# Performance work log

Measured on AMD Instinct MI355X. Metric: run time of the kernel, lower is better.

Reference implementation:

```python
import jax, jax.numpy as jnp
import numpy as np

T, B, D, H = 2048, 4, 1024, 16
DK = D // H
SCALE = 1.0 / np.sqrt(DK)


def setup_inputs() -> dict:
    key = jax.random.key(0)
    k1, k2, k3 = jax.random.split(key, 3)
    x = jax.random.normal(k1, (T, B, D), dtype=jnp.float32)
    # xavier_uniform-ish scaling
    W_qkv = jax.random.normal(k2, (3 * D, D), dtype=jnp.float32) * np.sqrt(2.0 / (D + 3 * D))
    W_out = jax.random.normal(k3, (D, D), dtype=jnp.float32) * np.sqrt(1.0 / D)
    b_out = jnp.zeros((D,), dtype=jnp.float32)
    return {"x": x, "W_qkv": W_qkv, "W_out": W_out, "b_out": b_out}


def reference(x, W_qkv, W_out, b_out):
    Tn, Bn, Dn = x.shape
    # QKV projection (Linear with weight [3D, D], no bias)
    qkv = x @ W_qkv.T                                  # (T, B, 3D)
    qkv = qkv.reshape(Tn, Bn, 3, H, DK)
    q, k, v = qkv[:, :, 0], qkv[:, :, 1], qkv[:, :, 2]  # each (T, B, H, dk)
    scores = jnp.einsum('tbhd,sbhd->bhts', q, k) * SCALE  # (B, H, T, T)
    causal = jnp.triu(jnp.ones((Tn, Tn), dtype=bool), k=1)
    scores = jnp.where(causal, -jnp.inf, scores)
    attn = jax.nn.softmax(scores, axis=-1)
    out = jnp.einsum('bhts,sbhd->tbhd', attn, v)        # (T, B, H, dk)
    out = out.reshape(Tn, Bn, Dn)
    return out @ W_out.T + b_out
```

## Files before the change

### kernel.cpp

```cpp
#include <hip/hip_runtime.h>
#include <stdint.h>

#define T_DIM 2048
#define B_DIM 4
#define D_DIM 1024
#define H_NUM 16
#define HD 64
#define MROWS (T_DIM * B_DIM)
#define QKV_N (3 * D_DIM)
#define ATT_C 0.18033688011112042f

typedef unsigned short u16;
typedef __bf16 bf16x8 __attribute__((ext_vector_type(8)));
typedef float f32x4 __attribute__((ext_vector_type(4)));
typedef float f32x16 __attribute__((ext_vector_type(16)));
typedef u16 u16x4 __attribute__((ext_vector_type(4)));
typedef u16 u16x8 __attribute__((ext_vector_type(8)));

__device__ __forceinline__ u16 f2bf(float f) {
  union { float f; unsigned u; } v; v.f = f;
  unsigned r = v.u + 0x7fffu + ((v.u >> 16) & 1u);
  return (u16)(r >> 16);
}

__device__ __forceinline__ void async_copy16(void* lds, const void* g) {
  __builtin_amdgcn_global_load_lds((__attribute__((address_space(1))) void*)(g),
                                   (__attribute__((address_space(3))) void*)(lds),
                                   16, 0, 0);
}

__global__ __launch_bounds__(256) void cast3_f32_bf16(
    const float* __restrict__ s0, const float* __restrict__ s1,
    const float* __restrict__ s2, u16* __restrict__ dst,
    int n0, int n01, int ntot4) {
  int i = blockIdx.x * 256 + threadIdx.x;
  if (i >= ntot4) return;
  int e = i * 4;
  const float* s; int off;
  if (e < n0) { s = s0; off = 0; }
  else if (e < n01) { s = s1; off = n0; }
  else { s = s2; off = n01; }
  float4 v = *reinterpret_cast<const float4*>(s + (e - off));
  u16x4 o = {f2bf(v.x), f2bf(v.y), f2bf(v.z), f2bf(v.w)};
  *reinterpret_cast<u16x4*>(dst + e) = o;
}

template <int OUT_F32_BIAS>
__global__ __launch_bounds__(256) void gemm_bt(
    const u16* __restrict__ A, const u16* __restrict__ Bm,
    u16* __restrict__ Cb, float* __restrict__ Cf, const float* __restrict__ bias,
    int M, int N, int K) {
  __shared__ __attribute__((aligned(16))) u16 As[128 * 64];
  __shared__ __attribute__((aligned(16))) u16 Bs[128 * 64];

  const int tid = threadIdx.x;
  const int lane = tid & 63, wid = tid >> 6;
  const int l15 = lane & 15, lg = lane >> 4;
  const int wr = wid >> 1, wc = wid & 1;
  const int m0 = blockIdx.y * 128, n0 = blockIdx.x * 128;

  f32x4 acc[4][4];
#pragma unroll
  for (int i = 0; i < 4; i++)
#pragma unroll
    for (int j = 0; j < 4; j++) acc[i][j] = (f32x4){0.f, 0.f, 0.f, 0.f};

  const int srow = tid >> 3;
  const int scol = (tid & 7) * 8;
  const u16* gA = A + (size_t)(m0 + srow) * K + scol;
  const u16* gB = Bm + (size_t)(n0 + srow) * K + scol;
  u16* lA = As + tid * 8;
  u16* lB = Bs + tid * 8;

  const int KT = K >> 6;
  for (int kt = 0; kt < KT; ++kt) {
    const int kofs = kt * 64;
#pragma unroll
    for (int p = 0; p < 4; ++p) {
      async_copy16(lA + p * 256 * 8, gA + (size_t)(p * 32) * K + kofs);
      async_copy16(lB + p * 256 * 8, gB + (size_t)(p * 32) * K + kofs);
    }
    __syncthreads();
#pragma unroll
    for (int kk = 0; kk < 2; ++kk) {
      bf16x8 af[4], bfr[4];
#pragma unroll
      for (int mt = 0; mt < 4; ++mt)
        af[mt] = *reinterpret_cast<const bf16x8*>(
            &As[(wr * 64 + mt * 16 + l15) * 64 + kk * 32 + lg * 8]);
#pragma unroll
      for (int nt = 0; nt < 4; ++nt)
        bfr[nt] = *reinterpret_cast<const bf16x8*>(
            &Bs[(wc * 64 + nt * 16 + l15) * 64 + kk * 32 + lg * 8]);
#pragma unroll
      for (int mt = 0; mt < 4; ++mt)
#pragma unroll
        for (int nt = 0; nt < 4; ++nt)
          acc[mt][nt] = __builtin_amdgcn_mfma_f32_16x16x32_bf16(
              af[mt], bfr[nt], acc[mt][nt], 0, 0, 0);
    }
    __syncthreads();
  }

#pragma unroll
  for (int mt = 0; mt < 4; ++mt) {
#pragma unroll
    for (int r = 0; r < 4; ++r) {
      const int row = m0 + wr * 64 + mt * 16 + lg * 4 + r;
#pragma unroll
      for (int nt = 0; nt < 4; ++nt) {
        const int col = n0 + wc * 64 + nt * 16 + l15;
        float v = acc[mt][nt][r];
        if (OUT_F32_BIAS) {
          Cf[(size_t)row * N + col] = v + bias[col];
        } else {
          Cb[(size_t)row * N + col] = f2bf(v);
        }
      }
    }
  }
}

__global__ __launch_bounds__(512, 1) void gemm_bt8_qkv(
    const u16* __restrict__ A, const u16* __restrict__ Bm,
    u16* __restrict__ Cb, int M, int N, int K) {
  extern __shared__ u16 sm[];

  const int tid = threadIdx.x;
  const int lane = tid & 63, wid = tid >> 6;
  const int wr = wid >> 2, wc = wid & 3;
  const int l15 = lane & 15, lg = lane >> 4;
  const int xr = ((l15 >> 2) & 1) << 4;

  const int nwg = gridDim.x * gridDim.y;
  const int lin = blockIdx.y * gridDim.x + blockIdx.x;
  const int swz = (lin & 7) * (nwg >> 3) + (lin >> 3);
  const int bx = swz % gridDim.x, by = swz / gridDim.x;
  const int m0 = by * 256, n0 = bx * 256;

  const int srow = tid >> 3;
  const int kxs = ((tid & 7) * 8) ^ (((tid >> 5) & 1) << 4);
  const u16* gA = A + (size_t)(m0 + srow) * K + kxs;
  const u16* gB = Bm + (size_t)(n0 + srow) * K + kxs;

#define STG(op_, h_, tk_, c_)                                                   \
  {                                                                             \
    const u16* g_ = ((op_) ? gB : gA) + (size_t)((h_) * 128) * K + (size_t)(tk_) * 64; \
    u16* d_ = sm + (c_) * 32768 + (op_) * 16384 + (h_) * 8192 + tid * 8;        \
    async_copy16(d_, g_);                                                       \
    async_copy16(d_ + 4096, g_ + (size_t)64 * K);                               \
  }

#define LDA_(mt_, kk_, c_)                                                      \
  (*reinterpret_cast<const bf16x8*>(sm + (c_) * 32768 + wr * 8192 +             \
      ((mt_) * 16 + l15) * 64 + (((kk_) * 32 + lg * 8) ^ xr)))
#define LDB_(nt_, kk_, c_)                                                      \
  (*reinterpret_cast<const bf16x8*>(sm + (c_) * 32768 + 16384 + (wc >> 1) * 8192 + \
      ((wc & 1) * 64 + (nt_) * 16 + l15) * 64 + (((kk_) * 32 + lg * 8) ^ xr)))

  f32x4 acc[8][4];
#pragma unroll
  for (int i = 0; i < 8; i++)
#pragma unroll
    for (int j = 0; j < 4; j++) acc[i][j] = (f32x4){0.f, 0.f, 0.f, 0.f};

  const int NT = K >> 6;

  STG(0, 0, 0, 0) STG(0, 1, 0, 0) STG(1, 0, 0, 0) STG(1, 1, 0, 0)
  STG(0, 0, 1, 1) STG(0, 1, 1, 1)
  asm volatile("s_waitcnt vmcnt(4)" ::: "memory");
  __builtin_amdgcn_sched_barrier(0);
  __builtin_amdgcn_s_barrier();

  for (int t = 0; t < NT; ++t) {
    const int c = t & 1;
    bf16x8 a03[4][2], a47[4][2], b01[2][2], b23[2][2];
#pragma unroll
    for (int mt = 0; mt < 4; ++mt) {
      a03[mt][0] = LDA_(mt, 0, c);
      a03[mt][1] = LDA_(mt, 1, c);
    }
#pragma unroll
    for (int nt = 0; nt < 2; ++nt) {
      b01[nt][0] = LDB_(nt, 0, c);
      b01[nt][1] = LDB_(nt, 1, c);
    }
    if (t + 1 < NT) STG(1, 0, t + 1, c ^ 1)
    __builtin_amdgcn_s_barrier();
    asm volatile("s_waitcnt lgkmcnt(0)" ::: "memory");
    __builtin_amdgcn_sched_barrier(0);
    __builtin_amdgcn_s_setprio(1);
#pragma unroll
    for (int mt = 0; mt < 4; ++mt)
#pragma unroll
      for (int nt = 0; nt < 2; ++nt)
#pragma unroll
        for (int kk = 0; kk < 2; ++kk)
          acc[mt][nt] = __builtin_amdgcn_mfma_f32_16x16x32_bf16(
              a03[mt][kk], b01[nt][kk], acc[mt][nt], 0, 0, 0);
    __builtin_amdgcn_s_setprio(0);
    __builtin_amdgcn_s_barrier();
#pragma unroll
    for (int mt = 0; mt < 4; ++mt) {
      a47[mt][0] = LDA_(mt + 4, 0, c);
      a47[mt][1] = LDA_(mt + 4, 1, c);
    }
    if (t + 1 < NT) STG(1, 1, t + 1, c ^ 1)
    __builtin_amdgcn_s_barrier();
    asm volatile("s_waitcnt lgkmcnt(0)" ::: "memory");
    __builtin_amdgcn_sched_barrier(0);
    __builtin_amdgcn_s_setprio(1);
#pragma unroll
    for (int mt = 0; mt < 4; ++mt)
#pragma unroll
      for (int nt = 0; nt < 2; ++nt)
#pragma unroll
        for (int kk = 0; kk < 2; ++kk)
          acc[mt + 4][nt] = __builtin_amdgcn_mfma_f32_16x16x32_bf16(
              a47[mt][kk], b01[nt][kk], acc[mt + 4][nt], 0, 0, 0);
    __builtin_amdgcn_s_setprio(0);
    __builtin_amdgcn_s_barrier();
#pragma unroll
    for (int nt = 0; nt < 2; ++nt) {
      b23[nt][0] = LDB_(nt + 2, 0, c);
      b23[nt][1] = LDB_(nt + 2, 1, c);
    }
    if (t + 2 < NT) STG(0, 0, t + 2, c)
    __builtin_amdgcn_s_barrier();
    asm volatile("s_waitcnt lgkmcnt(0)" ::: "memory");
    __builtin_amdgcn_sched_barrier(0);
    __builtin_amdgcn_s_setprio(1);
#pragma unroll
    for (int mt = 0; mt < 4; ++mt)
#pragma unroll
      for (int nt = 0; nt < 2; ++nt)
#pragma unroll
        for (int kk = 0; kk < 2; ++kk)
          acc[mt][nt + 2] = __builtin_amdgcn_mfma_f32_16x16x32_bf16(
              a03[mt][kk], b23[nt][kk], acc[mt][nt + 2], 0, 0, 0);
    __builtin_amdgcn_s_setprio(0);
    __builtin_amdgcn_s_barrier();
    if (t + 2 < NT) STG(0, 1, t + 2, c)
    __builtin_amdgcn_s_barrier();
    __builtin_amdgcn_s_setprio(1);
#pragma unroll
    for (int mt = 0; mt < 4; ++mt)
#pragma unroll
      for (int nt = 0; nt < 2; ++nt)
#pragma unroll
        for (int kk = 0; kk < 2; ++kk)
          acc[mt + 4][nt + 2] = __builtin_amdgcn_mfma_f32_16x16x32_bf16(
              a47[mt][kk], b23[nt][kk], acc[mt + 4][nt + 2], 0, 0, 0);
    __builtin_amdgcn_s_setprio(0);
    if (t + 1 < NT) {
      if (t + 2 < NT) {
        asm volatile("s_waitcnt vmcnt(4)" ::: "memory");
      } else {
        asm volatile("s_waitcnt vmcnt(0)" ::: "memory");
      }
      __builtin_amdgcn_sched_barrier(0);
    }
    __builtin_amdgcn_s_barrier();
  }

  const float qsc = (n0 < D_DIM) ? ATT_C : 1.0f;
#pragma unroll
  for (int mt = 0; mt < 8; ++mt) {
#pragma unroll
    for (int r = 0; r < 4; ++r) {
      const int row = m0 + wr * 128 + mt * 16 + lg * 4 + r;
#pragma unroll
      for (int nt = 0; nt < 4; ++nt) {
        const int col = n0 + wc * 64 + nt * 16 + l15;
        Cb[(size_t)row * N + col] = f2bf(acc[mt][nt][r] * qsc);
      }
    }
  }
#undef STG
#undef LDA_
#undef LDB_
}

#define VF_STRIDE 24
#define VF_FRAG (32 * VF_STRIDE)

__device__ __forceinline__ void process32(
    const bf16x8 (&qf)[4], f32x16 (&o)[2], f32x16& lacc,
    int q0w, int kv0, int l31, int hi, bool needMask, const bf16x8 onesf,
    const u16* __restrict__ Ks, const u16* __restrict__ Vf) {
  f32x16 s[2];
#pragma unroll
  for (int kb = 0; kb < 2; ++kb)
#pragma unroll
    for (int r = 0; r < 16; ++r) s[kb][r] = 0.f;

  __builtin_amdgcn_s_setprio(1);
#pragma unroll
  for (int kb = 0; kb < 2; ++kb) {
#pragma unroll
    for (int ks = 0; ks < 4; ++ks) {
      const int row = kb * 32 + l31;
      bf16x8 kf = *reinterpret_cast<const bf16x8*>(
          &Ks[row * 64 + ((((ks << 1) | hi)) ^ (l31 & 7)) * 8]);
      s[kb] = __builtin_amdgcn_mfma_f32_32x32x16_bf16(kf, qf[ks], s[kb], 0, 0, 0);
    }
  }
  __builtin_amdgcn_s_setprio(0);

  if (needMask) {
    const int q = q0w + l31;
#pragma unroll
    for (int kb = 0; kb < 2; ++kb)
#pragma unroll
      for (int r = 0; r < 16; ++r) {
        const int kv = kv0 + kb * 32 + (r & 3) + ((r >> 2) << 3) + (hi << 2);
        if (kv > q) s[kb][r] = -1e30f;
      }
  }
#pragma unroll
  for (int kb = 0; kb < 2; ++kb)
#pragma unroll
    for (int r = 0; r < 16; ++r)
      s[kb][r] = __builtin_amdgcn_exp2f(s[kb][r]);

  union Frag { unsigned u[4]; bf16x8 v; };
  Frag pf[4];
#pragma unroll
  for (int kb = 0; kb < 2; ++kb)
#pragma unroll
    for (int g = 0; g < 2; ++g) {
#pragma unroll
      for (int t2 = 0; t2 < 2; ++t2) {
        unsigned x, y;
        asm("v_cvt_pk_bf16_f32 %0, %1, %2"
            : "=v"(x) : "v"(s[kb][g * 8 + t2 * 2]), "v"(s[kb][g * 8 + t2 * 2 + 1]));
        asm("v_cvt_pk_bf16_f32 %0, %1, %2"
            : "=v"(y) : "v"(s[kb][g * 8 + t2 * 2 + 4]), "v"(s[kb][g * 8 + t2 * 2 + 5]));
        asm("v_permlane32_swap_b32 %0, %1" : "+v"(x), "+v"(y));
        pf[kb * 2 + g].u[t2] = x;
        pf[kb * 2 + g].u[t2 + 2] = y;
      }
    }

  __builtin_amdgcn_s_setprio(1);
#pragma unroll
  for (int ks = 0; ks < 4; ++ks) {
    lacc = __builtin_amdgcn_mfma_f32_32x32x16_bf16(onesf, pf[ks].v, lacc, 0, 0, 0);
#pragma unroll
    for (int db = 0; db < 2; ++db) {
      bf16x8 vf = *reinterpret_cast<const bf16x8*>(
          &Vf[(ks * 2 + db) * VF_FRAG + l31 * VF_STRIDE + hi * 8]);
      o[db] = __builtin_amdgcn_mfma_f32_32x32x16_bf16(vf, pf[ks].v, o[db], 0, 0, 0);
    }
  }
  __builtin_amdgcn_s_setprio(0);
}

__global__ __launch_bounds__(256, 2) void attn_kernel(
    const u16* __restrict__ qkv, u16* __restrict__ aout) {
  __shared__ __attribute__((aligned(16))) u16 Ks[128 * 64];
  __shared__ __attribute__((aligned(16))) u16 Vf[16 * VF_FRAG];

  const int tid = threadIdx.x;
  const int lane = tid & 63, w = tid >> 6;
  const int l31 = lane & 31, hi = lane >> 5;

  const int nwg = gridDim.x * gridDim.y;
  const int lin = blockIdx.y * gridDim.x + blockIdx.x;
  const int swz = (lin & 7) * (nwg >> 3) + (lin >> 3);
  const int px = swz % gridDim.x;
  const int bh = swz / gridDim.x;
  const int b = bh >> 4, h = bh & 15;
  const int qtA = px, qtB = 15 - px;
  const int q0A = qtA * 128 + w * 32, q0B = qtB * 128 + w * 32;

  bf16x8 qfA[4], qfB[4];
  {
    const u16* pA = qkv + ((size_t)(q0A + l31) * B_DIM + b) * QKV_N + h * HD + hi * 8;
    const u16* pB = qkv + ((size_t)(q0B + l31) * B_DIM + b) * QKV_N + h * HD + hi * 8;
#pragma unroll
    for (int ks = 0; ks < 4; ++ks) {
      qfA[ks] = *reinterpret_cast<const bf16x8*>(pA + ks * 16);
      qfB[ks] = *reinterpret_cast<const bf16x8*>(pB + ks * 16);
    }
  }

  bf16x8 onesf;
  {
    union { u16 u[8]; bf16x8 v; } ou;
#pragma unroll
    for (int i = 0; i < 8; ++i) ou.u[i] = 0x3F80;
    onesf = ou.v;
  }

  f32x16 oA[2], oB[2], laccA, laccB;
#pragma unroll
  for (int r = 0; r < 16; ++r) { laccA[r] = 0.f; laccB[r] = 0.f; }
#pragma unroll
  for (int db = 0; db < 2; ++db)
#pragma unroll
    for (int r = 0; r < 16; ++r) { oA[db][r] = 0.f; oB[db][r] = 0.f; }

  const int srow = tid >> 3;
  const int scol = (tid & 7) * 8;
  const int csw = (tid & 7) ^ (srow & 7);

  for (int kt2 = 0; kt2 <= qtB; ++kt2) {
    const int base = kt2 * 128;
#pragma unroll
    for (int p = 0; p < 4; ++p) {
      const u16* gK = qkv + ((size_t)(base + p * 32 + srow) * B_DIM + b) * QKV_N +
                      D_DIM + h * HD + csw * 8;
      async_copy16(Ks + tid * 8 + p * 2048, gK);
    }
    u16x8 vv[4];
#pragma unroll
    for (int p = 0; p < 4; ++p) {
      const u16* gV = qkv + ((size_t)(base + p * 32 + srow) * B_DIM + b) * QKV_N +
                      2 * D_DIM + h * HD + scol;
      vv[p] = *reinterpret_cast<const u16x8*>(gV);
    }
#pragma unroll
    for (int p = 0; p < 4; ++p) {
      const int kvl = p * 32 + srow;
      const int fb = (kvl >> 4) * 2;
      const int e16 = kvl & 15;
#pragma unroll
      for (int jj = 0; jj < 8; ++jj) {
        const int j = (jj + srow) & 7;
        const int d = scol + j;
        Vf[(fb + (d >> 5)) * VF_FRAG + (d & 31) * VF_STRIDE + e16] = vv[p][j];
      }
    }
    __syncthreads();

#pragma unroll
    for (int half = 0; half < 2; ++half) {
      const int kv0 = base + half * 64;
      const u16* Kh = Ks + half * (64 * 64);
      const u16* Vh = Vf + half * 8 * VF_FRAG;
      if (kv0 <= q0A + 31)
        process32(qfA, oA, laccA, q0A, kv0, l31, hi, kv0 + 63 > q0A, onesf, Kh, Vh);
      if (kv0 <= q0B + 31)
        process32(qfB, oB, laccB, q0B, kv0, l31, hi, kv0 + 63 > q0B, onesf, Kh, Vh);
    }
    __syncthreads();
  }

#pragma unroll
  for (int t = 0; t < 2; ++t) {
    const float inv = 1.0f / (t == 0 ? laccA[0] : laccB[0]);
    const int q0w = t == 0 ? q0A : q0B;
    f32x16* o = t == 0 ? oA : oB;
    u16* orow = aout + ((size_t)(q0w + l31) * B_DIM + b) * D_DIM + h * HD;
#pragma unroll
    for (int db = 0; db < 2; ++db)
#pragma unroll
      for (int rq = 0; rq < 4; ++rq) {
        u16x4 o4;
#pragma unroll
        for (int e = 0; e < 4; ++e) o4[e] = f2bf(o[db][rq * 4 + e] * inv);
        *reinterpret_cast<u16x4*>(orow + db * 32 + rq * 8 + hi * 4) = o4;
      }
  }
}

extern "C" void kernel_launch(void* const* d_in, const int* in_sizes, int n_in,
                              void* d_out, int out_size, void* d_ws, size_t ws_size,
                              hipStream_t stream) {
  (void)in_sizes; (void)n_in; (void)out_size; (void)ws_size;
  const float* x = (const float*)d_in[0];
  const float* Wqkv = (const float*)d_in[1];
  const float* Wout = (const float*)d_in[2];
  const float* bout = (const float*)d_in[3];
  float* out = (float*)d_out;

  u16* xb = (u16*)d_ws;
  u16* wqkvb = xb + (size_t)MROWS * D_DIM;
  u16* woutb = wqkvb + (size_t)QKV_N * D_DIM;
  u16* qkv = woutb + (size_t)D_DIM * D_DIM;
  u16* aout = qkv + (size_t)MROWS * QKV_N;

  {
    const int n0 = MROWS * D_DIM;
    const int n01 = n0 + QKV_N * D_DIM;
    const int ntot = n01 + D_DIM * D_DIM;
    const int n4 = ntot / 4;
    cast3_f32_bf16<<<(n4 + 255) / 256, 256, 0, stream>>>(
        x, Wqkv, Wout, xb, n0, n01, n4);
  }

  hipFuncSetAttribute((const void*)gemm_bt8_qkv,
                      hipFuncAttributeMaxDynamicSharedMemorySize, 131072);
  gemm_bt8_qkv<<<dim3(QKV_N / 256, MROWS / 256), 512, 131072, stream>>>(
      xb, wqkvb, qkv, MROWS, QKV_N, D_DIM);

  attn_kernel<<<dim3(8, B_DIM * H_NUM), 256, 0, stream>>>(qkv, aout);

  gemm_bt<1><<<dim3(D_DIM / 128, MROWS / 128), 256, 0, stream>>>(
      aout, woutb, nullptr, out, bout, MROWS, D_DIM, D_DIM);
}
```

Before: 189.7 us.

## Split KV tiles across two wave groups per attention block and merge partials

```diff
diff --git a/kernel.cpp b/kernel.cpp
--- a/kernel.cpp
+++ b/kernel.cpp
@@ -150,7 +150,6 @@
     async_copy16(d_, g_);                                                       \
     async_copy16(d_ + 4096, g_ + (size_t)64 * K);                               \
   }
-
 #define LDA_(mt_, kk_, c_)                                                      \
   (*reinterpret_cast<const bf16x8*>(sm + (c_) * 32768 + wr * 8192 +             \
       ((mt_) * 16 + l15) * 64 + (((kk_) * 32 + lg * 8) ^ xr)))
@@ -283,6 +282,8 @@
 
 #define VF_STRIDE 24
 #define VF_FRAG (32 * VF_STRIDE)
+#define KS_U16 8192
+#define GRP_U16 (KS_U16 + 16 * VF_FRAG)
 
 __device__ __forceinline__ void process32(
     const bf16x8 (&qf)[4], f32x16 (&o)[2], f32x16& lacc,
@@ -356,13 +357,14 @@
   __builtin_amdgcn_s_setprio(0);
 }
 
-__global__ __launch_bounds__(256, 2) void attn_kernel(
+__global__ __launch_bounds__(512, 4) void attn_kernel(
     const u16* __restrict__ qkv, u16* __restrict__ aout) {
-  __shared__ __attribute__((aligned(16))) u16 Ks[128 * 64];
-  __shared__ __attribute__((aligned(16))) u16 Vf[16 * VF_FRAG];
+  extern __shared__ __attribute__((aligned(16))) u16 smA[];
 
   const int tid = threadIdx.x;
   const int lane = tid & 63, w = tid >> 6;
+  const int g = w >> 2, wl = w & 3;
+  const int ltid = tid & 255;
   const int l31 = lane & 31, hi = lane >> 5;
 
   const int nwg = gridDim.x * gridDim.y;
@@ -372,7 +374,10 @@
   const int bh = swz / gridDim.x;
   const int b = bh >> 4, h = bh & 15;
   const int qtA = px, qtB = 15 - px;
-  const int q0A = qtA * 128 + w * 32, q0B = qtB * 128 + w * 32;
+  const int q0A = qtA * 128 + wl * 32, q0B = qtB * 128 + wl * 32;
+
+  u16* Ks = smA + g * GRP_U16;
+  u16* Vf = Ks + KS_U16;
 
   bf16x8 qfA[4], qfB[4];
   {
@@ -401,67 +406,101 @@
 #pragma unroll
     for (int r = 0; r < 16; ++r) { oA[db][r] = 0.f; oB[db][r] = 0.f; }
 
-  const int srow = tid >> 3;
-  const int scol = (tid & 7) * 8;
-  const int csw = (tid & 7) ^ (srow & 7);
-
-  for (int kt2 = 0; kt2 <= qtB; ++kt2) {
+  const int srow = ltid >> 3;
+  const int scol = (ltid & 7) * 8;
+  const int csw = (ltid & 7) ^ (srow & 7);
+
+  const int ntiles = qtB + 1;
+  const int iters = (ntiles + 1) >> 1;
+  for (int it = 0; it < iters; ++it) {
+    const int kt2 = 2 * it + g;
+    const bool active = kt2 < ntiles;
     const int base = kt2 * 128;
-#pragma unroll
-    for (int p = 0; p < 4; ++p) {
-      const u16* gK = qkv + ((size_t)(base + p * 32 + srow) * B_DIM + b) * QKV_N +
-                      D_DIM + h * HD + csw * 8;
-      async_copy16(Ks + tid * 8 + p * 2048, gK);
-    }
-    u16x8 vv[4];
-#pragma unroll
-    for (int p = 0; p < 4; ++p) {
-      const u16* gV = qkv + ((size_t)(base + p * 32 + srow) * B_DIM + b) * QKV_N +
-                      2 * D_DIM + h * HD + scol;
-      vv[p] = *reinterpret_cast<const u16x8*>(gV);
-    }
-#pragma unroll
-    for (int p = 0; p < 4; ++p) {
-      const int kvl = p * 32 + srow;
-      const int fb = (kvl >> 4) * 2;
-      const int e16 = kvl & 15;
-#pragma unroll
-      for (int jj = 0; jj < 8; ++jj) {
-        const int j = (jj + srow) & 7;
-        const int d = scol + j;
-        Vf[(fb + (d >> 5)) * VF_FRAG + (d & 31) * VF_STRIDE + e16] = vv[p][j];
+    if (active) {
+#pragma unroll
+      for (int p = 0; p < 4; ++p) {
+        const u16* gK = qkv + ((size_t)(base + p * 32 + srow) * B_DIM + b) * QKV_N +
+                        D_DIM + h * HD + csw * 8;
+        async_copy16(Ks + ltid * 8 + p * 2048, gK);
+      }
+      u16x8 vv[4];
+#pragma unroll
+      for (int p = 0; p < 4; ++p) {
+        const u16* gV = qkv + ((size_t)(base + p * 32 + srow) * B_DIM + b) * QKV_N +
+                        2 * D_DIM + h * HD + scol;
+        vv[p] = *reinterpret_cast<const u16x8*>(gV);
+      }
+#pragma unroll
+      for (int p = 0; p < 4; ++p) {
+        const int kvl = p * 32 + srow;
+        const int fb = (kvl >> 4) * 2;
+        const int e16 = kvl & 15;
+#pragma unroll
+        for (int jj = 0; jj < 8; ++jj) {
+          const int j = (jj + srow) & 7;
+          const int d = scol + j;
+          Vf[(fb + (d >> 5)) * VF_FRAG + (d & 31) * VF_STRIDE + e16] = vv[p][j];
+        }
       }
     }
     __syncthreads();
-
-#pragma unroll
-    for (int half = 0; half < 2; ++half) {
-      const int kv0 = base + half * 64;
-      const u16* Kh = Ks + half * (64 * 64);
-      const u16* Vh = Vf + half * 8 * VF_FRAG;
-      if (kv0 <= q0A + 31)
-        process32(qfA, oA, laccA, q0A, kv0, l31, hi, kv0 + 63 > q0A, onesf, Kh, Vh);
-      if (kv0 <= q0B + 31)
-        process32(qfB, oB, laccB, q0B, kv0, l31, hi, kv0 + 63 > q0B, onesf, Kh, Vh);
+    if (active) {
+#pragma unroll
+      for (int half = 0; half < 2; ++half) {
+        const int kv0 = base + half * 64;
+        const u16* Kh = Ks + half * (64 * 64);
+        const u16* Vh = Vf + half * 8 * VF_FRAG;
+        if (kv0 <= q0A + 31)
+          process32(qfA, oA, laccA, q0A, kv0, l31, hi, kv0 + 63 > q0A, onesf, Kh, Vh);
+        if (kv0 <= q0B + 31)
+          process32(qfB, oB, laccB, q0B, kv0, l31, hi, kv0 + 63 > q0B, onesf, Kh, Vh);
+      }
     }
     __syncthreads();
   }
 
-#pragma unroll
-  for (int t = 0; t < 2; ++t) {
-    const float inv = 1.0f / (t == 0 ? laccA[0] : laccB[0]);
-    const int q0w = t == 0 ? q0A : q0B;
-    f32x16* o = t == 0 ? oA : oB;
-    u16* orow = aout + ((size_t)(q0w + l31) * B_DIM + b) * D_DIM + h * HD;
-#pragma unroll
-    for (int db = 0; db < 2; ++db)
-#pragma unroll
-      for (int rq = 0; rq < 4; ++rq) {
-        u16x4 o4;
-#pragma unroll
-        for (int e = 0; e < 4; ++e) o4[e] = f2bf(o[db][rq * 4 + e] * inv);
-        *reinterpret_cast<u16x4*>(orow + db * 32 + rq * 8 + hi * 4) = o4;
-      }
+  float* mb = (float*)smA;
+#define MPASS(vec_)                                                            \
+  __syncthreads();                                                             \
+  if (g == 1) {                                                                \
+    _Pragma("unroll") for (int r = 0; r < 16; ++r)                             \
+        mb[r * 256 + wl * 64 + lane] = vec_[r];                                \
+  }                                                                            \
+  __syncthreads();                                                             \
+  if (g == 0) {                                                                \
+    _Pragma("unroll") for (int r = 0; r < 16; ++r)                             \
+        vec_[r] += mb[r * 256 + wl * 64 + lane];                               \
+  }
+  MPASS(oA[0]) MPASS(oA[1]) MPASS(oB[0]) MPASS(oB[1])
+  __syncthreads();
+  if (g == 1) {
+    mb[wl * 64 + lane] = laccA[0];
+    mb[256 + wl * 64 + lane] = laccB[0];
+  }
+  __syncthreads();
+  if (g == 0) {
+    laccA[0] += mb[wl * 64 + lane];
+    laccB[0] += mb[256 + wl * 64 + lane];
+  }
+#undef MPASS
+
+  if (g == 0) {
+#pragma unroll
+    for (int t = 0; t < 2; ++t) {
+      const float inv = 1.0f / (t == 0 ? laccA[0] : laccB[0]);
+      const int q0w = t == 0 ? q0A : q0B;
+      f32x16* o = t == 0 ? oA : oB;
+      u16* orow = aout + ((size_t)(q0w + l31) * B_DIM + b) * D_DIM + h * HD;
+#pragma unroll
+      for (int db = 0; db < 2; ++db)
+#pragma unroll
+        for (int rq = 0; rq < 4; ++rq) {
+          u16x4 o4;
+#pragma unroll
+          for (int e = 0; e < 4; ++e) o4[e] = f2bf(o[db][rq * 4 + e] * inv);
+          *reinterpret_cast<u16x4*>(orow + db * 32 + rq * 8 + hi * 4) = o4;
+        }
+    }
   }
 }
 
@@ -495,7 +534,9 @@
   gemm_bt8_qkv<<<dim3(QKV_N / 256, MROWS / 256), 512, 131072, stream>>>(
       xb, wqkvb, qkv, MROWS, QKV_N, D_DIM);
 
-  attn_kernel<<<dim3(8, B_DIM * H_NUM), 256, 0, stream>>>(qkv, aout);
+  hipFuncSetAttribute((const void*)attn_kernel,
+                      hipFuncAttributeMaxDynamicSharedMemorySize, 2 * GRP_U16 * 2);
+  attn_kernel<<<dim3(8, B_DIM * H_NUM), 512, 2 * GRP_U16 * 2, stream>>>(qkv, aout);
 
   gemm_bt<1><<<dim3(D_DIM / 128, MROWS / 128), 256, 0, stream>>>(
       aout, woutb, nullptr, out, bout, MROWS, D_DIM, D_DIM);
```

New measurement: 468.2 us. +146.8%, slower.
